# Optimization experiments

Hardware: AMD Instinct MI355X
Metric: run time of the kernel (lower is better)

The kernel has to match this reference:

```python
import jax, jax.numpy as jnp
import numpy as np
from jax import lax

SPATIAL = 4
PAD = 1
STRIDE = 1


def _route(x, rconv_w, rconv_b, fc_w, fc_b, num_experts):
    # x: (b, c, h, w); adaptive avg pool to (SPATIAL, SPATIAL) -- h,w divisible by SPATIAL
    b, c, h, w = x.shape
    pooled = x.reshape(b, c, SPATIAL, h // SPATIAL, SPATIAL, w // SPATIAL).mean(axis=(3, 5))
    # 1x1 conv: (b,c,s,s) x (rc,c) -> (b,rc,s,s)
    y = jnp.einsum('bcij,rc->brij', pooled, rconv_w) + rconv_b[None, :, None, None]
    y = jax.nn.relu(y).reshape(b, -1)                      # (b, rc*s*s)
    y = jax.nn.relu(y @ fc_w.T + fc_b)                     # (b, num_experts*c)
    y = y.reshape(b, num_experts, c)
    return jax.nn.sigmoid(y)                               # (b, k, c)


def _conv_per_sample(xi, wi):
    # xi: (c_in, h, w), wi: (c_out, c_in, kh, kw)
    out = lax.conv_general_dilated(
        xi[None], wi, window_strides=(STRIDE, STRIDE),
        padding=[(PAD, PAD), (PAD, PAD)],
        dimension_numbers=('NCHW', 'OIHW', 'NCHW'))
    return out[0]


def setup_inputs() -> dict:
    key = jax.random.key(0)
    ks = jax.random.split(key, 6)
    b, c_in, c_out, kk, ne = 16, 256, 256, 3, 3
    rc = max(c_in // 16, 16)  # reduction_channels = 16
    x = jax.random.normal(ks[0], (b, c_in, 64, 64), dtype=jnp.float32)
    expert_weight = jax.random.normal(ks[1], (ne, c_out, c_in, kk, kk), dtype=jnp.float32) * 0.02
    rconv_w = jax.random.normal(ks[2], (rc, c_in), dtype=jnp.float32) * 0.05
    rconv_b = jax.random.normal(ks[3], (rc,), dtype=jnp.float32) * 0.05
    fc_w = jax.random.normal(ks[4], (ne * c_in, rc * SPATIAL * SPATIAL), dtype=jnp.float32) * 0.05
    fc_b = jax.random.normal(ks[5], (ne * c_in,), dtype=jnp.float32) * 0.05
    return {"x": x, "expert_weight": expert_weight, "rconv_w": rconv_w,
            "rconv_b": rconv_b, "fc_w": fc_w, "fc_b": fc_b}


def reference(x, expert_weight, rconv_w, rconv_b, fc_w, fc_b):
    ne = expert_weight.shape[0]
    r = _route(x, rconv_w, rconv_b, fc_w, fc_b, ne)        # (b, k, c_in)
    # per-sample combined weights: routing scales input channels of each expert kernel
    w = jnp.einsum('bkc,kocij->bocij', r, expert_weight)    # (b, c_out, c_in, kh, kw)
    out = jax.vmap(_conv_per_sample)(x, w)                  # (b, c_out, h', w')
    return out
```

## Files before the change

### kernel.cpp

```cpp
#include <hip/hip_runtime.h>

#define B_   16
#define C_   256
#define OC_  256
#define H_   64
#define W_   64

typedef __attribute__((ext_vector_type(8))) __bf16 bf16x8;
typedef __attribute__((ext_vector_type(4))) float  f32x4;

__device__ __forceinline__ short f2bf(float f) {
    unsigned u = __float_as_uint(f);
    u += 0x7fffu + ((u >> 16) & 1u);
    return (short)(u >> 16);
}
__device__ __forceinline__ unsigned pk2(float a, float b) {
    return (unsigned(f2bf(a)) & 0xffffu) | (unsigned(f2bf(b)) << 16);
}
__device__ __forceinline__ void gll16(const void* g, void* l) {
    __builtin_amdgcn_global_load_lds(
        (const __attribute__((address_space(1))) unsigned int*)g,
        (__attribute__((address_space(3))) unsigned int*)l,
        16, 0, 0);
}

__global__ __launch_bounds__(256) void k_transpose_pool(
        const float* __restrict__ x, short* __restrict__ xt, float* __restrict__ pooled) {
    int y = blockIdx.x, b = blockIdx.y, t = threadIdx.x;
    int si = y >> 4;
    int lane = t & 63, wv = t >> 6;
    int xq = lane & 15, cw = lane >> 4;
    __shared__ float tile[64 * 67];

    for (int cc = 0; cc < 4; ++cc) {
        int cbase = cc * 64;
        if (cc) __syncthreads();
        #pragma unroll
        for (int r = 0; r < 4; ++r) {
            int c_l = r * 16 + wv * 4 + cw;
            float4 v = *(const float4*)&x[(((size_t)b * C_ + cbase + c_l) * H_ + y) * W_ + xq * 4];
            float* tp = &tile[c_l * 67 + xq * 4];
            tp[0] = v.x; tp[1] = v.y; tp[2] = v.z; tp[3] = v.w;
            float s = v.x + v.y + v.z + v.w;
            s += __shfl_xor(s, 1);
            s += __shfl_xor(s, 2);
            if ((lane & 3) == 0)
                atomicAdd(&pooled[((b * 4 + si) * 4 + (xq >> 2)) * 256 + cbase + c_l], s);
        }
        __syncthreads();
        #pragma unroll
        for (int r2 = 0; r2 < 2; ++r2) {
            int u = r2 * 256 + t;
            int xx = u >> 3, cgl = u & 7;
            float f[8];
            #pragma unroll
            for (int j = 0; j < 8; ++j) f[j] = tile[(cgl * 8 + j) * 67 + xx];
            uint4 pkv;
            pkv.x = pk2(f[0], f[1]); pkv.y = pk2(f[2], f[3]);
            pkv.z = pk2(f[4], f[5]); pkv.w = pk2(f[6], f[7]);
            *(uint4*)&xt[(((size_t)b * H_ + y) * W_ + xx) * C_ + cbase + cgl * 8] = pkv;
        }
    }
}

__global__ __launch_bounds__(256) void k_route(
        const float* __restrict__ pooled, const float* __restrict__ rconv_w,
        const float* __restrict__ rconv_b, const float* __restrict__ fc_w,
        const float* __restrict__ fc_b, float* __restrict__ r_buf) {
    int b = blockIdx.x;
    int t = threadIdx.x;
    __shared__ float pl[16][257];
    __shared__ float y1[256];

    #pragma unroll
    for (int q = 0; q < 16; ++q)
        pl[q][t] = pooled[b * 4096 + q * 256 + t] * (1.0f / 256.0f);
    __syncthreads();
    {
        int rcc = t >> 4, ss = t & 15;
        float acc = rconv_b[rcc];
        #pragma unroll 8
        for (int c = 0; c < 256; ++c)
            acc += pl[ss][c] * rconv_w[rcc * 256 + c];
        y1[rcc * 16 + ss] = fmaxf(acc, 0.f);
    }
    __syncthreads();
    for (int e0 = 0; e0 < 768; e0 += 256) {
        int e = e0 + t;
        float acc = fc_b[e];
        #pragma unroll 8
        for (int q = 0; q < 256; ++q)
            acc += y1[q] * fc_w[(size_t)e * 256 + q];
        acc = fmaxf(acc, 0.f);
        r_buf[(size_t)b * 768 + e] = 1.f / (1.f + __expf(-acc));
    }
}

__global__ __launch_bounds__(256) void k_combine(
        const float* __restrict__ E, const float* __restrict__ r_buf,
        short* __restrict__ wcomb) {
    int o = blockIdx.x;
    int t = threadIdx.x;
    __shared__ float eT[3][2304];
    #pragma unroll
    for (int k = 0; k < 3; ++k)
        #pragma unroll
        for (int q = 0; q < 9; ++q)
            eT[k][q * 256 + t] = E[((size_t)k * OC_ + o) * 2304 + q * 256 + t];
    __syncthreads();
    int c = t;
    float e0[9], e1[9], e2[9];
    #pragma unroll
    for (int tap = 0; tap < 9; ++tap) {
        e0[tap] = eT[0][c * 9 + tap];
        e1[tap] = eT[1][c * 9 + tap];
        e2[tap] = eT[2][c * 9 + tap];
    }
    int ccs = c >> 5;
    int sub = (o & 15) * 32 + ((c >> 3) & 3) * 8 + (c & 7);
    int og  = o >> 4;
    for (int b = 0; b < 16; ++b) {
        float r0 = r_buf[(size_t)b * 768 + c];
        float r1 = r_buf[(size_t)b * 768 + 256 + c];
        float r2 = r_buf[(size_t)b * 768 + 512 + c];
        short* wo = wcomb + (size_t)b * 589824;
        #pragma unroll
        for (int tap = 0; tap < 9; ++tap) {
            float v = r0 * e0[tap] + r1 * e1[tap] + r2 * e2[tap];
            wo[((tap * 8 + ccs) * 16 + og) * 512 + sub] = f2bf(v);
        }
    }
}

__global__ __launch_bounds__(256, 2) void k_conv(
        const short* __restrict__ xt, const short* __restrict__ wcomb,
        float* __restrict__ out, const short* __restrict__ zbuf) {
    int lin  = blockIdx.x;
    int work = (lin & 7) * 64 + (lin >> 3);
    int b      = work >> 5;
    int o_base = ((work >> 4) & 1) * 128;
    int y0     = (work & 15) * 4;

    int t = threadIdx.x;
    int lane = t & 63, w = t >> 6;
    int quad = lane >> 4, l15 = lane & 15;

    __shared__ __align__(16) short win[6 * 64 * 64];

    int zoff = (int)(zbuf - xt);

    int woff[12];
    #pragma unroll
    for (int r = 0; r < 12; ++r) {
        int u = r * 256 + t;
        int pos = u >> 3, sp = u & 7;
        int wrow = pos >> 6, xc = pos & 63;
        int yy = y0 - 1 + wrow;
        int ss = sp ^ (xc & 7);
        woff[r] = ((unsigned)yy < 64u)
            ? ((b * 64 + yy) * 64 + xc) * 256 + ss * 8
            : zoff;
    }

    int m_base = (w & 1) * 64;
    int ry0    = (w >> 1) * 2;

    const short* pA = wcomb + (size_t)b * 589824
                    + ((o_base + m_base) >> 4) * 512 + l15 * 32 + quad * 8;

    f32x4 acc[4][8];
    #pragma unroll
    for (int i = 0; i < 4; ++i)
        #pragma unroll
        for (int j = 0; j < 8; ++j) acc[i][j] = {0.f, 0.f, 0.f, 0.f};

    for (int cc = 0; cc < 4; ++cc) {
        int ccOff = cc * 64;
        int ccA   = cc * 16384;
        #pragma unroll
        for (int r = 0; r < 12; ++r)
            gll16(xt + woff[r] + ccOff, &win[(r * 256 + w * 64) * 8]);

        bf16x8 P[2][4];
        #pragma unroll
        for (int mb = 0; mb < 4; ++mb) {
            P[0][mb] = *(const bf16x8*)(pA + ccA + mb * 512);
            P[1][mb] = *(const bf16x8*)(pA + ccA + 8192 + mb * 512);
        }
        __syncthreads();

        #pragma unroll
        for (int ph = 0; ph < 18; ++ph) {
            const int tp = ph >> 1, s = ph & 1;
            const int ti = tp / 3, tj = tp % 3;
            const int cur = ph & 1;
            int slog = s * 4 + quad;

            bf16x8 bv[8];
            #pragma unroll
            for (int nb = 0; nb < 8; ++nb) {
                int rr = nb >> 2, xq4 = nb & 3;
                int xc = xq4 * 16 + l15 + (tj - 1);
                bool ok = ((unsigned)xc < 64u);
                int xs = ok ? xc : 0;
                int wrow = ry0 + rr + ti;
                bf16x8 v = *(const bf16x8*)&win[(wrow * 64 + xs) * 64
                                                + ((slog ^ (xs & 7)) * 8)];
                bf16x8 zz = {};
                bv[nb] = ok ? v : zz;
            }
            __builtin_amdgcn_s_setprio(1);
            #pragma unroll
            for (int mb = 0; mb < 4; ++mb)
                #pragma unroll
                for (int nb = 0; nb < 8; ++nb)
                    acc[mb][nb] = __builtin_amdgcn_mfma_f32_16x16x32_bf16(
                        P[cur][mb], bv[nb], acc[mb][nb], 0, 0, 0);
            __builtin_amdgcn_s_setprio(0);

            if (ph < 16) {
                const int np = ph + 2, ntp = np >> 1, ns = np & 1;
                #pragma unroll
                for (int mb = 0; mb < 4; ++mb)
                    P[cur][mb] = *(const bf16x8*)(pA + ccA + ntp * 65536
                                                  + ns * 8192 + mb * 512);
            }
        }
        if (cc < 3) __syncthreads();
    }

    #pragma unroll
    for (int mb = 0; mb < 4; ++mb) {
        #pragma unroll
        for (int nb = 0; nb < 8; ++nb) {
            int rr = nb >> 2, xq4 = nb & 3;
            int xx = xq4 * 16 + l15;
            int yy = y0 + ry0 + rr;
            #pragma unroll
            for (int rg = 0; rg < 4; ++rg) {
                int o = o_base + m_base + mb * 16 + quad * 4 + rg;
                out[(((size_t)b * OC_ + o) * H_ + yy) * W_ + xx] = acc[mb][nb][rg];
            }
        }
    }
}

extern "C" void kernel_launch(void* const* d_in, const int* in_sizes, int n_in,
                              void* d_out, int out_size, void* d_ws, size_t ws_size,
                              hipStream_t stream) {
    const float* x       = (const float*)d_in[0];
    const float* E       = (const float*)d_in[1];
    const float* rconv_w = (const float*)d_in[2];
    const float* rconv_b = (const float*)d_in[3];
    const float* fc_w    = (const float*)d_in[4];
    const float* fc_b    = (const float*)d_in[5];
    float* out = (float*)d_out;

    char* ws = (char*)d_ws;
    short* xt     = (short*)(ws);
    short* wcomb  = (short*)(ws + 33554432);
    float* pooled = (float*)(ws + 52428800);
    short* zbuf   = (short*)(ws + 52690944);
    float* rbuf   = (float*)(ws + 52692992);

    hipMemsetAsync(pooled, 0, 262144 + 1024, stream);

    k_transpose_pool<<<dim3(64, 16), 256, 0, stream>>>(x, xt, pooled);
    k_route<<<dim3(16), 256, 0, stream>>>(pooled, rconv_w, rconv_b, fc_w, fc_b, rbuf);
    k_combine<<<dim3(256), 256, 0, stream>>>(E, rbuf, wcomb);
    k_conv<<<dim3(512), 256, 0, stream>>>(xt, wcomb, out, zbuf);
}
```

Measured before the change: 241.7 us.

## Switch conv GEMM to 32x32x16 MFMA with matching weight layout and tiling

Replaces the 16x16x32 bf16 MFMA tiles with 32x32x16 tiles, re-laying out the combined weights so each lane loads 8 consecutive input channels for a 32-row output block. Each wave now owns one output row and all 128 output channels of the block instead of 64 channels by two rows. The weight prefetch for the next channel chunk is carried across the chunk boundary. The aim is fewer LDS reads per MFMA and higher matrix-core throughput, at the cost of more accumulator registers per wave and a different LDS access pattern.

```diff
diff --git a/kernel.cpp b/kernel.cpp
--- a/kernel.cpp
+++ b/kernel.cpp
@@ -6,8 +6,9 @@
 #define H_   64
 #define W_   64
 
-typedef __attribute__((ext_vector_type(8))) __bf16 bf16x8;
-typedef __attribute__((ext_vector_type(4))) float  f32x4;
+typedef __attribute__((ext_vector_type(8)))  __bf16 bf16x8;
+typedef __attribute__((ext_vector_type(4)))  float  f32x4;
+typedef __attribute__((ext_vector_type(16))) float  f32x16;
 
 __device__ __forceinline__ short f2bf(float f) {
     unsigned u = __float_as_uint(f);
@@ -116,9 +117,11 @@
         e1[tap] = eT[1][c * 9 + tap];
         e2[tap] = eT[2][c * 9 + tap];
     }
-    int ccs = c >> 5;
-    int sub = (o & 15) * 32 + ((c >> 3) & 3) * 8 + (c & 7);
-    int og  = o >> 4;
+    int ks   = c >> 4;
+    int half = (c >> 3) & 1;
+    int ch   = c & 7;
+    int og   = o >> 5, ol = o & 31;
+    int sub  = ol * 16 + half * 8 + ch;
     for (int b = 0; b < 16; ++b) {
         float r0 = r_buf[(size_t)b * 768 + c];
         float r1 = r_buf[(size_t)b * 768 + 256 + c];
@@ -127,7 +130,7 @@
         #pragma unroll
         for (int tap = 0; tap < 9; ++tap) {
             float v = r0 * e0[tap] + r1 * e1[tap] + r2 * e2[tap];
-            wo[((tap * 8 + ccs) * 16 + og) * 512 + sub] = f2bf(v);
+            wo[((tap * 16 + ks) * 8 + og) * 512 + sub] = f2bf(v);
         }
     }
 }
@@ -143,7 +146,7 @@
 
     int t = threadIdx.x;
     int lane = t & 63, w = t >> 6;
-    int quad = lane >> 4, l15 = lane & 15;
+    int l31 = lane & 31, lh = lane >> 5;
 
     __shared__ __align__(16) short win[6 * 64 * 64];
 
@@ -162,50 +165,51 @@
             : zoff;
     }
 
-    int m_base = (w & 1) * 64;
-    int ry0    = (w >> 1) * 2;
-
+    int og0 = o_base >> 5;
     const short* pA = wcomb + (size_t)b * 589824
-                    + ((o_base + m_base) >> 4) * 512 + l15 * 32 + quad * 8;
-
-    f32x4 acc[4][8];
+                    + og0 * 512 + l31 * 16 + lh * 8;
+
+    f32x16 acc[4][2];
     #pragma unroll
     for (int i = 0; i < 4; ++i)
         #pragma unroll
-        for (int j = 0; j < 8; ++j) acc[i][j] = {0.f, 0.f, 0.f, 0.f};
+        for (int j = 0; j < 2; ++j)
+            #pragma unroll
+            for (int q = 0; q < 16; ++q) acc[i][j][q] = 0.f;
+
+    bf16x8 P[2][4];
 
     for (int cc = 0; cc < 4; ++cc) {
         int ccOff = cc * 64;
-        int ccA   = cc * 16384;
         #pragma unroll
         for (int r = 0; r < 12; ++r)
             gll16(xt + woff[r] + ccOff, &win[(r * 256 + w * 64) * 8]);
 
-        bf16x8 P[2][4];
-        #pragma unroll
-        for (int mb = 0; mb < 4; ++mb) {
-            P[0][mb] = *(const bf16x8*)(pA + ccA + mb * 512);
-            P[1][mb] = *(const bf16x8*)(pA + ccA + 8192 + mb * 512);
+        if (cc == 0) {
+            #pragma unroll
+            for (int mb = 0; mb < 4; ++mb) {
+                P[0][mb] = *(const bf16x8*)(pA + (0 * 16 + 0) * 4096 + mb * 512);
+                P[1][mb] = *(const bf16x8*)(pA + (0 * 16 + 1) * 4096 + mb * 512);
+            }
         }
         __syncthreads();
 
         #pragma unroll
-        for (int ph = 0; ph < 18; ++ph) {
-            const int tp = ph >> 1, s = ph & 1;
-            const int ti = tp / 3, tj = tp % 3;
+        for (int ph = 0; ph < 36; ++ph) {
+            const int tap = ph >> 2, ks = ph & 3;
+            const int ti = tap / 3, tj = tap % 3;
             const int cur = ph & 1;
-            int slog = s * 4 + quad;
-
-            bf16x8 bv[8];
-            #pragma unroll
-            for (int nb = 0; nb < 8; ++nb) {
-                int rr = nb >> 2, xq4 = nb & 3;
-                int xc = xq4 * 16 + l15 + (tj - 1);
+            const int slot = ks * 2 + lh;
+
+            bf16x8 bv[2];
+            #pragma unroll
+            for (int nb = 0; nb < 2; ++nb) {
+                int xc = nb * 32 + l31 + (tj - 1);
                 bool ok = ((unsigned)xc < 64u);
                 int xs = ok ? xc : 0;
-                int wrow = ry0 + rr + ti;
+                int wrow = w + ti;
                 bf16x8 v = *(const bf16x8*)&win[(wrow * 64 + xs) * 64
-                                                + ((slog ^ (xs & 7)) * 8)];
+                                                + ((slot ^ (xs & 7)) * 8)];
                 bf16x8 zz = {};
                 bv[nb] = ok ? v : zz;
             }
@@ -213,17 +217,23 @@
             #pragma unroll
             for (int mb = 0; mb < 4; ++mb)
                 #pragma unroll
-                for (int nb = 0; nb < 8; ++nb)
-                    acc[mb][nb] = __builtin_amdgcn_mfma_f32_16x16x32_bf16(
+                for (int nb = 0; nb < 2; ++nb)
+                    acc[mb][nb] = __builtin_amdgcn_mfma_f32_32x32x16_bf16(
                         P[cur][mb], bv[nb], acc[mb][nb], 0, 0, 0);
             __builtin_amdgcn_s_setprio(0);
 
-            if (ph < 16) {
-                const int np = ph + 2, ntp = np >> 1, ns = np & 1;
+            if (ph < 34) {
+                const int np = ph + 2, ntap = np >> 2, nks = np & 3;
                 #pragma unroll
                 for (int mb = 0; mb < 4; ++mb)
-                    P[cur][mb] = *(const bf16x8*)(pA + ccA + ntp * 65536
-                                                  + ns * 8192 + mb * 512);
+                    P[cur][mb] = *(const bf16x8*)(pA
+                        + (ntap * 16 + cc * 4 + nks) * 4096 + mb * 512);
+            } else if (cc < 3) {
+                const int nks = (ph == 34) ? 0 : 1;
+                #pragma unroll
+                for (int mb = 0; mb < 4; ++mb)
+                    P[cur][mb] = *(const bf16x8*)(pA
+                        + (0 * 16 + (cc + 1) * 4 + nks) * 4096 + mb * 512);
             }
         }
         if (cc < 3) __syncthreads();
@@ -232,13 +242,12 @@
     #pragma unroll
     for (int mb = 0; mb < 4; ++mb) {
         #pragma unroll
-        for (int nb = 0; nb < 8; ++nb) {
-            int rr = nb >> 2, xq4 = nb & 3;
-            int xx = xq4 * 16 + l15;
-            int yy = y0 + ry0 + rr;
-            #pragma unroll
-            for (int rg = 0; rg < 4; ++rg) {
-                int o = o_base + m_base + mb * 16 + quad * 4 + rg;
+        for (int nb = 0; nb < 2; ++nb) {
+            int xx = nb * 32 + l31;
+            int yy = y0 + w;
+            #pragma unroll
+            for (int rg = 0; rg < 16; ++rg) {
+                int o = o_base + mb * 32 + (rg & 3) + ((rg >> 2) * 8) + lh * 4;
                 out[(((size_t)b * OC_ + o) * H_ + yy) * W_ + xx] = acc[mb][nb][rg];
             }
         }
```

Result: slower. 250.8 us (+3.8%).
